# Kernel optimization log

Measured on AMD Instinct MI355X. Metric: run time of the kernel, lower is better.

The kernel has to match this reference:

```python
import jax, jax.numpy as jnp
import numpy as np

Q_LO, Q_HI = 0.15, 0.85   # quantiles from __init__ q=(0.15, 0.85)
Z_INDEX = 0.0             # Z_index=0 -> mask = outside [q_lo, q_hi]
Z_SIMPLE = 1.0            # Z_index_simple fallback


def _nn_diff(S1, S2):
    # For each point in S1, signed per-coordinate residual to its nearest
    # neighbor in S2 (brute-force cdist + argmin + gather). S1:[N,3] S2:[M,3]
    d2 = (jnp.sum(S1 * S1, -1)[:, None] + jnp.sum(S2 * S2, -1)[None, :]
          - 2.0 * (S1 @ S2.T))              # [N, M] squared distances
    idx = jnp.argmin(d2, axis=1)            # nearest index in S2, [N]
    return S1 - S2[idx]                     # [N, 3]


def _robust_masked_std(x):
    # torch: quantile-based outlier mask (no_grad), then unbiased std of
    # the masked elements. Implemented with mask weights so shapes are static.
    xf = x.reshape(-1)
    xs = jax.lax.stop_gradient(xf)
    qs = jnp.quantile(xs, jnp.array([Q_LO, Q_HI], dtype=xs.dtype))
    iqr = qs[1] - qs[0]
    mask = (xs < qs[0] - Z_INDEX * iqr) | (xs > qs[1] + Z_INDEX * iqr)
    # fallback chain matching torch edge cases: simple |x-mean|>Z*std, then all
    mu, sd = xs.mean(), xs.std(ddof=1)
    simple = jnp.abs(xs - mu) > Z_SIMPLE * sd
    simple = jnp.where(simple.sum() > 0, simple, jnp.ones_like(simple))
    w = jnp.where(mask.sum() > 0, mask, simple).astype(xf.dtype)
    cnt = w.sum()
    mean_w = jnp.sum(w * xf) / cnt
    var = jnp.sum(w * (xf - mean_w) ** 2) / (cnt - 1.0)  # unbiased (torch.std)
    return jnp.sqrt(var)


def _sigma_max(S1, S2):
    s1 = _robust_masked_std(_nn_diff(S1, S2))  # std of S1->S2 residuals
    s2 = _robust_masked_std(_nn_diff(S2, S1))  # std of S2->S1 residuals
    return jnp.maximum(s1, s2)                 # max(self.sigma_distance(...))


def setup_inputs() -> dict:
    key = jax.random.key(0)
    k1, k2 = jax.random.split(key)
    B, N, M, D = 16, 4096, 4096, 3
    x = jax.random.uniform(k1, (B, N, D), dtype=jnp.float32)
    y = jax.random.uniform(k2, (B, M, D), dtype=jnp.float32)
    return {"x": x, "y": y}


def reference(x, y):
    per_batch = jax.vmap(_sigma_max)(x, y)  # [B]
    return per_batch.mean()
```

## Files before the change

### kernel.cpp

```cpp
#include <hip/hip_runtime.h>
#include <stdint.h>
#include <math.h>

typedef unsigned short u16;
typedef unsigned long long ull;

#define NPTS  4096
#define NB    16
#define NRES  12288
#define NPAIR 32
#define G     16
#define NCELL 4096
#define HCEL  0.0625f
#define SSTR  4160
#define MARGIN 1e-5f
#define RANK_LO 1843u
#define RANK_HI 10443u

__device__ __forceinline__ uint32_t f2key(float f) {
    uint32_t u = __float_as_uint(f);
    return (u & 0x80000000u) ? ~u : (u | 0x80000000u);
}
__device__ __forceinline__ float key2f(uint32_t k) {
    uint32_t u = (k & 0x80000000u) ? (k ^ 0x80000000u) : ~k;
    return __uint_as_float(u);
}

__global__ __launch_bounds__(1024) void build_kernel(const float* __restrict__ x,
                                                     const float* __restrict__ y,
                                                     float4* __restrict__ arrA,
                                                     u16* __restrict__ starts,
                                                     u16* __restrict__ idx16,
                                                     unsigned int* __restrict__ counters) {
    __shared__ uint32_t hist[NCELL];
    __shared__ uint32_t wpart[16];
    const int pd = blockIdx.x, b = pd >> 1, dir = pd & 1;
    const float* t = (dir == 0 ? y : x) + (size_t)b * NPTS * 3;
    const int tid = threadIdx.x, lane = tid & 63, wv = tid >> 6;

    #pragma unroll
    for (int j = 0; j < 4; ++j) hist[tid * 4 + j] = 0u;
    if (pd == 0 && tid == 0) counters[0] = 0u;
    __syncthreads();

    float f[12];
    int ci[4];
    {
        const float4* tp = reinterpret_cast<const float4*>(t + (size_t)tid * 12);
        #pragma unroll
        for (int j = 0; j < 3; ++j) {
            const float4 v = tp[j];
            f[j * 4 + 0] = v.x; f[j * 4 + 1] = v.y; f[j * 4 + 2] = v.z; f[j * 4 + 3] = v.w;
        }
        #pragma unroll
        for (int k = 0; k < 4; ++k) {
            const int cx = (int)(f[k * 3 + 0] * 16.f);
            const int cy = (int)(f[k * 3 + 1] * 16.f);
            const int cz = (int)(f[k * 3 + 2] * 16.f);
            ci[k] = (cx * G + cy) * G + cz;
            atomicAdd(&hist[ci[k]], 1u);
        }
    }
    __syncthreads();

    {
        uint32_t loc[4], sum = 0;
        const int base = tid * 4;
        #pragma unroll
        for (int j = 0; j < 4; ++j) { loc[j] = hist[base + j]; sum += loc[j]; }
        uint32_t sc = sum;
        #pragma unroll
        for (int off = 1; off < 64; off <<= 1) {
            const uint32_t u = __shfl_up(sc, off);
            if (lane >= off) sc += u;
        }
        if (lane == 63) wpart[wv] = sc;
        __syncthreads();
        uint32_t wbase = 0;
        #pragma unroll
        for (int k = 0; k < 16; ++k) wbase += (k < wv) ? wpart[k] : 0u;
        uint32_t ex = wbase + sc - sum;
        #pragma unroll
        for (int j = 0; j < 4; ++j) { hist[base + j] = ex; ex += loc[j]; }
    }
    __syncthreads();

    for (int i = tid; i <= NCELL; i += 1024)
        starts[(size_t)pd * SSTR + i] = (u16)((i == NCELL) ? NPTS : hist[i]);
    __syncthreads();

    #pragma unroll
    for (int k = 0; k < 4; ++k) {
        const float px = f[k * 3 + 0], py = f[k * 3 + 1], pz = f[k * 3 + 2];
        const uint32_t pos = atomicAdd(&hist[ci[k]], 1u);
        const float w = fmaf(pz, pz, fmaf(py, py, px * px));
        arrA[(size_t)pd * NPTS + pos] = make_float4(-2.f * px, -2.f * py, -2.f * pz, w);
        idx16[(size_t)pd * NPTS + pos] = (u16)(tid * 4 + k);
    }
}

__global__ __launch_bounds__(256, 8) void query_kernel(const float4* __restrict__ arrA,
                                                       const u16* __restrict__ starts,
                                                       const u16* __restrict__ idx16,
                                                       uint32_t* __restrict__ keys,
                                                       double* __restrict__ partials) {
    __shared__ double wred[8];
    const int pd = blockIdx.y;
    const int tid = threadIdx.x, lane = tid & 63, wv = tid >> 6;
    const int l4 = tid & 3;
    const int p = blockIdx.x * 64 + (tid >> 2);

    const float4* __restrict__ tp = arrA + (size_t)pd * NPTS;
    const u16* __restrict__ st = starts + (size_t)pd * SSTR;
    const u16* __restrict__ ixp = idx16 + (size_t)pd * NPTS;

    const float4 Q = arrA[(size_t)(pd ^ 1) * NPTS + p];
    const float qx = -0.5f * Q.x, qy = -0.5f * Q.y, qz = -0.5f * Q.z;
    const float qq = Q.w;
    const int cx = (int)(qx * 16.f), cy = (int)(qy * 16.f), cz = (int)(qz * 16.f);

    float best = 3.0e38f;
    ull pk = ~0ull;

    #define SCAN_RUN(A_, E_)                                                        \
        for (int p2 = (A_) + l4; p2 < (E_); p2 += 4) {                              \
            const float4 T = tp[p2];                                                \
            const float d = fmaf(qx, T.x, fmaf(qy, T.y, fmaf(qz, T.z, T.w)));       \
            best = fminf(best, d);                                                  \
            const ull cand = ((ull)f2key(d) << 32) |                                \
                             ((ull)ixp[p2] << 16) | (uint32_t)p2;                   \
            pk = (cand < pk) ? cand : pk;                                           \
        }

    {
        const int zlo = max(cz - 1, 0), zhi = min(cz + 1, G - 1);
        int a9[9], e9[9];
        #pragma unroll
        for (int r = 0; r < 9; ++r) {
            const int ix = min(max(cx + (r / 3) - 1, 0), G - 1);
            const int iy = min(max(cy + (r % 3) - 1, 0), G - 1);
            const int c0 = (ix * G + iy) * G;
            a9[r] = st[c0 + zlo];
            e9[r] = st[c0 + zhi + 1];
        }
        #pragma unroll
        for (int r = 0; r < 9; ++r) SCAN_RUN(a9[r], e9[r])
    }

    for (int s = 2; s <= G - 1; ++s) {
        float qb = best;
        qb = fminf(qb, __shfl_xor(qb, 1));
        qb = fminf(qb, __shfl_xor(qb, 2));
        const float dmin = (float)(s - 1) * HCEL;
        if (fmaf(dmin, dmin, -(qb + qq)) > MARGIN) break;
        for (int dx = -s; dx <= s; ++dx) {
            const int ix = cx + dx;
            if (ix < 0 || ix > G - 1) continue;
            const int adx = dx < 0 ? -dx : dx;
            for (int dy = -s; dy <= s; ++dy) {
                const int iy = cy + dy;
                if (iy < 0 || iy > G - 1) continue;
                const int ady = dy < 0 ? -dy : dy;
                const int c0 = (ix * G + iy) * G;
                if (max(adx, ady) == s) {
                    const int zl = max(cz - s, 0), zh = min(cz + s, G - 1);
                    const int a = st[c0 + zl], e = st[c0 + zh + 1];
                    SCAN_RUN(a, e)
                } else {
                    const int z1 = cz - s;
                    if (z1 >= 0) { const int a = st[c0 + z1], e = st[c0 + z1 + 1]; SCAN_RUN(a, e) }
                    const int z2 = cz + s;
                    if (z2 <= G - 1) { const int a = st[c0 + z2], e = st[c0 + z2 + 1]; SCAN_RUN(a, e) }
                }
            }
        }
    }
    #undef SCAN_RUN

    {
        ull o = __shfl_xor(pk, 1); pk = (o < pk) ? o : pk;
        o = __shfl_xor(pk, 2);     pk = (o < pk) ? o : pk;
    }

    const int pos = (int)(pk & 0xFFFFull);
    const float4 T = tp[pos];
    const float rx = qx - (-0.5f * T.x);
    const float ry = qy - (-0.5f * T.y);
    const float rz = qz - (-0.5f * T.z);

    if (l4 < 3) {
        const uint32_t kk = (l4 == 0) ? f2key(rx) : ((l4 == 1) ? f2key(ry) : f2key(rz));
        keys[(size_t)pd * NRES + (size_t)p * 3 + l4] = kk;
    }

    double s1 = 0.0, s2 = 0.0;
    if (l4 == 0) {
        s1 = (double)rx + (double)ry + (double)rz;
        s2 = (double)rx * rx + (double)ry * ry + (double)rz * rz;
    }
    #pragma unroll
    for (int off = 32; off; off >>= 1) { s1 += __shfl_down(s1, off); s2 += __shfl_down(s2, off); }
    if (lane == 0) { wred[wv] = s1; wred[4 + wv] = s2; }
    __syncthreads();
    if (tid == 0) {
        double a = 0.0, c = 0.0;
        for (int k = 0; k < 4; ++k) { a += wred[k]; c += wred[4 + k]; }
        partials[(size_t)pd * 128 + blockIdx.x + 0]  = a;
        partials[(size_t)pd * 128 + 64 + blockIdx.x] = c;
    }
}

template <int BPT>
__device__ __forceinline__ void scanB(uint32_t* h, uint32_t* wtmp) {
    const int tid = threadIdx.x, lane = tid & 63, wv = tid >> 6;
    const int base = tid * BPT;
    uint32_t loc[BPT], sum = 0;
    #pragma unroll
    for (int j = 0; j < BPT; ++j) { loc[j] = h[base + j]; sum += loc[j]; }
    uint32_t sc = sum;
    #pragma unroll
    for (int off = 1; off < 64; off <<= 1) {
        const uint32_t u = __shfl_up(sc, off);
        if (lane >= off) sc += u;
    }
    if (lane == 63) wtmp[wv] = sc;
    __syncthreads();
    uint32_t wb = 0;
    #pragma unroll
    for (int k = 0; k < 16; ++k) wb += (k < wv) ? wtmp[k] : 0u;
    uint32_t ex = wb + sc - sum;
    #pragma unroll
    for (int j = 0; j < BPT; ++j) { h[base + j] = ex; ex += loc[j]; }
    __syncthreads();
}

template <int BPT>
__device__ __forceinline__ void psearchB(const uint32_t* h, int n, uint32_t r,
                                         uint32_t total, uint32_t* out3) {
    const int base = threadIdx.x * BPT;
    #pragma unroll
    for (int j = 0; j < BPT; ++j) {
        const int i = base + j;
        if (i < n) {
            const uint32_t lo = h[i];
            const uint32_t hi = (i + 1 < n) ? h[i + 1] : total;
            if (lo <= r && r < hi) { out3[0] = (uint32_t)i; out3[1] = lo; out3[2] = hi; }
        }
    }
}

__global__ __launch_bounds__(1024) void sigma_kernel(const uint32_t* __restrict__ keysg,
                                                     const double* __restrict__ partials,
                                                     float* __restrict__ sig,
                                                     unsigned int* __restrict__ counters,
                                                     float* __restrict__ out) {
    __shared__ uint32_t hist[4096];
    __shared__ uint32_t wtmp[16];
    __shared__ uint32_t bc[12];
    __shared__ double dr[64];
    __shared__ int io[32];
    __shared__ uint32_t um[32];

    const int pair = blockIdx.x;
    const int tid = threadIdx.x, lane = tid & 63, wv = tid >> 6;

    uint32_t key[12];
    const uint32_t* kp = keysg + (size_t)pair * NRES;
    #pragma unroll
    for (int e = 0; e < 12; ++e) key[e] = kp[e * 1024 + tid];

    {
        double a = (tid < 128) ? partials[(size_t)pair * 128 + tid] : 0.0;
        #pragma unroll
        for (int off = 32; off; off >>= 1) a += __shfl_down(a, off);
        if (lane == 0 && wv < 2) dr[wv] = a;
    }
    __syncthreads();
    const double S = dr[0], S2 = dr[1];
    const double mu = S / NRES;
    const double var_all = (S2 - S * mu) / (NRES - 1);
    const double sd = sqrt(var_all > 0.0 ? var_all : 0.0);
    __syncthreads();

    hist[tid * 2] = 0u; hist[tid * 2 + 1] = 0u;
    __syncthreads();
    #pragma unroll
    for (int e = 0; e < 12; ++e) atomicAdd(&hist[key[e] >> 21], 1u);
    __syncthreads();
    scanB<2>(hist, wtmp);
    psearchB<2>(hist, 2048, RANK_LO, NRES, bc + 0);
    psearchB<2>(hist, 2048, RANK_HI, NRES, bc + 3);
    __syncthreads();
    const uint32_t pA1 = bc[0], rA1 = RANK_LO - bc[1], totA1 = bc[2] - bc[1];
    const uint32_t pB1 = bc[3], rB1 = RANK_HI - bc[4], totB1 = bc[5] - bc[4];
    __syncthreads();

    #pragma unroll
    for (int j = 0; j < 4; ++j) hist[tid * 4 + j] = 0u;
    __syncthreads();
    #pragma unroll
    for (int e = 0; e < 12; ++e) {
        const uint32_t k = key[e];
        const uint32_t pfx = k >> 21, bin = (k >> 10) & 2047u;
        if (pfx == pA1) atomicAdd(&hist[bin], 1u);
        if (pfx == pB1) atomicAdd(&hist[2048 + bin], 1u);
    }
    __syncthreads();
    scanB<2>(hist, wtmp);
    scanB<2>(hist + 2048, wtmp);
    psearchB<2>(hist, 2048, rA1, totA1, bc + 0);
    psearchB<2>(hist + 2048, 2048, rB1, totB1, bc + 3);
    __syncthreads();
    const uint32_t pA2 = (pA1 << 11) | bc[0], rA2 = rA1 - bc[1], totA2 = bc[2] - bc[1];
    const uint32_t pB2 = (pB1 << 11) | bc[3], rB2 = rB1 - bc[4], totB2 = bc[5] - bc[4];
    __syncthreads();

    hist[tid * 2] = 0u; hist[tid * 2 + 1] = 0u;
    __syncthreads();
    #pragma unroll
    for (int e = 0; e < 12; ++e) {
        const uint32_t k = key[e];
        if ((k >> 10) == pA2) atomicAdd(&hist[k & 1023u], 1u);
        if ((k >> 10) == pB2) atomicAdd(&hist[1024 + (k & 1023u)], 1u);
    }
    __syncthreads();
    scanB<1>(hist, wtmp);
    scanB<1>(hist + 1024, wtmp);
    psearchB<1>(hist, 1024, rA2, totA2, bc + 0);
    psearchB<1>(hist + 1024, 1024, rB2, totB2, bc + 3);
    __syncthreads();
    const uint32_t k0 = (pA2 << 10) | bc[0];
    const uint32_t k2 = (pB2 << 10) | bc[3];
    const bool dup1 = (bc[2] >= rA2 + 2u);
    const bool dup3 = (bc[5] >= rB2 + 2u);

    uint32_t m1 = 0xFFFFFFFFu, m3 = 0xFFFFFFFFu;
    #pragma unroll
    for (int e = 0; e < 12; ++e) {
        const uint32_t k = key[e];
        if (k > k0 && k < m1) m1 = k;
        if (k > k2 && k < m3) m3 = k;
    }
    {
        uint32_t a = m1, c = m3;
        #pragma unroll
        for (int off = 32; off; off >>= 1) {
            const uint32_t ua = __shfl_down(a, off), uc = __shfl_down(c, off);
            a = (ua < a) ? ua : a; c = (uc < c) ? uc : c;
        }
        if (lane == 0) { um[wv] = a; um[16 + wv] = c; }
    }
    __syncthreads();
    uint32_t m1r = 0xFFFFFFFFu, m3r = 0xFFFFFFFFu;
    for (int k = 0; k < 16; ++k) {
        m1r = (um[k] < m1r) ? um[k] : m1r;
        m3r = (um[16 + k] < m3r) ? um[16 + k] : m3r;
    }
    const uint32_t k1 = dup1 ? k0 : m1r;
    const uint32_t k3 = dup3 ? k2 : m3r;

    const double vl0 = (double)key2f(k0), vl1 = (double)key2f(k1);
    const double vh0 = (double)key2f(k2), vh1 = (double)key2f(k3);
    const double fr_lo = 0.15 * (NRES - 1) - (double)RANK_LO;
    const double fr_hi = 0.85 * (NRES - 1) - (double)RANK_HI;
    const float q_lo = (float)(vl0 + fr_lo * (vl1 - vl0));
    const float q_hi = (float)(vh0 + fr_hi * (vh1 - vh0));

    int cq = 0, cs = 0;
    double sq = 0.0, ss = 0.0, sqq = 0.0, ssq = 0.0;
    #pragma unroll
    for (int e = 0; e < 12; ++e) {
        const float f = key2f(key[e]);
        const double fd = (double)f;
        if ((f < q_lo) || (f > q_hi)) { cq++; sq += fd; sqq += fd * fd; }
        if (fabs(fd - mu) > sd)       { cs++; ss += fd; ssq += fd * fd; }
    }
    {
        double a0 = sq, a1 = ss, a2 = sqq, a3 = ssq;
        int b0 = cq, b1 = cs;
        #pragma unroll
        for (int off = 32; off; off >>= 1) {
            a0 += __shfl_down(a0, off); a1 += __shfl_down(a1, off);
            a2 += __shfl_down(a2, off); a3 += __shfl_down(a3, off);
            b0 += __shfl_down(b0, off); b1 += __shfl_down(b1, off);
        }
        if (lane == 0) {
            dr[wv] = a0; dr[16 + wv] = a1; dr[32 + wv] = a2; dr[48 + wv] = a3;
            io[wv] = b0; io[16 + wv] = b1;
        }
    }
    __syncthreads();
    if (tid == 0) {
        double sq_t = 0, ss_t = 0, sqq_t = 0, ssq_t = 0;
        int cq_t = 0, cs_t = 0;
        for (int k = 0; k < 16; ++k) {
            sq_t += dr[k]; ss_t += dr[16 + k]; sqq_t += dr[32 + k]; ssq_t += dr[48 + k];
            cq_t += io[k]; cs_t += io[16 + k];
        }
        double cnt, sum, sumsq;
        if (cq_t > 0)      { cnt = cq_t;  sum = sq_t; sumsq = sqq_t; }
        else if (cs_t > 0) { cnt = cs_t;  sum = ss_t; sumsq = ssq_t; }
        else               { cnt = NRES;  sum = S;    sumsq = S2; }
        const double mean_w = sum / cnt;
        const double var = (sumsq - cnt * mean_w * mean_w) / (cnt - 1.0);
        const float sv = (float)sqrt(var > 0.0 ? var : 0.0);

        __hip_atomic_store(&sig[pair], sv, __ATOMIC_RELEASE, __HIP_MEMORY_SCOPE_AGENT);
        const unsigned prev = __hip_atomic_fetch_add(&counters[0], 1u,
                                                     __ATOMIC_ACQ_REL,
                                                     __HIP_MEMORY_SCOPE_AGENT);
        if (prev == NPAIR - 1) {
            float m = 0.f;
            for (int i = 0; i < NB; ++i) {
                const float s0 = __hip_atomic_load(&sig[2 * i], __ATOMIC_ACQUIRE,
                                                   __HIP_MEMORY_SCOPE_AGENT);
                const float s1v = __hip_atomic_load(&sig[2 * i + 1], __ATOMIC_ACQUIRE,
                                                    __HIP_MEMORY_SCOPE_AGENT);
                m += fmaxf(s0, s1v);
            }
            out[0] = m / (float)NB;
        }
    }
}

extern "C" void kernel_launch(void* const* d_in, const int* in_sizes, int n_in,
                              void* d_out, int out_size, void* d_ws, size_t ws_size,
                              hipStream_t stream) {
    const float* x = (const float*)d_in[0];
    const float* y = (const float*)d_in[1];
    char* w = (char*)d_ws;
    float4*       arrA     = (float4*)(w);
    uint32_t*     keys     = (uint32_t*)(w + 2097152);
    double*       partials = (double*)(w + 3670016);
    float*        sig      = (float*)(w + 3702784);
    unsigned int* counters = (unsigned int*)(w + 3702912);
    u16*          starts   = (u16*)(w + 3703040);
    u16*          idx16    = (u16*)(w + 3969280);

    build_kernel<<<NPAIR, 1024, 0, stream>>>(x, y, arrA, starts, idx16, counters);
    query_kernel<<<dim3(64, NPAIR), 256, 0, stream>>>(arrA, starts, idx16,
                                                      keys, partials);
    sigma_kernel<<<NPAIR, 1024, 0, stream>>>(keys, partials, sig, counters,
                                             (float*)d_out);
}
```

Measured before the change: 111.9 us.

## Flatten 3x3 neighbor runs into one strided loop and drop original-index tiebreak

```diff
diff --git a/kernel.cpp b/kernel.cpp
--- a/kernel.cpp
+++ b/kernel.cpp
@@ -30,7 +30,6 @@
                                                      const float* __restrict__ y,
                                                      float4* __restrict__ arrA,
                                                      u16* __restrict__ starts,
-                                                     u16* __restrict__ idx16,
                                                      unsigned int* __restrict__ counters) {
     __shared__ uint32_t hist[NCELL];
     __shared__ uint32_t wpart[16];
@@ -95,13 +94,11 @@
         const uint32_t pos = atomicAdd(&hist[ci[k]], 1u);
         const float w = fmaf(pz, pz, fmaf(py, py, px * px));
         arrA[(size_t)pd * NPTS + pos] = make_float4(-2.f * px, -2.f * py, -2.f * pz, w);
-        idx16[(size_t)pd * NPTS + pos] = (u16)(tid * 4 + k);
     }
 }
 
 __global__ __launch_bounds__(256, 8) void query_kernel(const float4* __restrict__ arrA,
                                                        const u16* __restrict__ starts,
-                                                       const u16* __restrict__ idx16,
                                                        uint32_t* __restrict__ keys,
                                                        double* __restrict__ partials) {
     __shared__ double wred[8];
@@ -112,47 +109,59 @@
 
     const float4* __restrict__ tp = arrA + (size_t)pd * NPTS;
     const u16* __restrict__ st = starts + (size_t)pd * SSTR;
-    const u16* __restrict__ ixp = idx16 + (size_t)pd * NPTS;
 
     const float4 Q = arrA[(size_t)(pd ^ 1) * NPTS + p];
     const float qx = -0.5f * Q.x, qy = -0.5f * Q.y, qz = -0.5f * Q.z;
     const float qq = Q.w;
     const int cx = (int)(qx * 16.f), cy = (int)(qy * 16.f), cz = (int)(qz * 16.f);
 
-    float best = 3.0e38f;
     ull pk = ~0ull;
 
-    #define SCAN_RUN(A_, E_)                                                        \
-        for (int p2 = (A_) + l4; p2 < (E_); p2 += 4) {                              \
-            const float4 T = tp[p2];                                                \
-            const float d = fmaf(qx, T.x, fmaf(qy, T.y, fmaf(qz, T.z, T.w)));       \
-            best = fminf(best, d);                                                  \
-            const ull cand = ((ull)f2key(d) << 32) |                                \
-                             ((ull)ixp[p2] << 16) | (uint32_t)p2;                   \
-            pk = (cand < pk) ? cand : pk;                                           \
-        }
-
     {
         const int zlo = max(cz - 1, 0), zhi = min(cz + 1, G - 1);
-        int a9[9], e9[9];
-        #pragma unroll
-        for (int r = 0; r < 9; ++r) {
-            const int ix = min(max(cx + (r / 3) - 1, 0), G - 1);
-            const int iy = min(max(cy + (r % 3) - 1, 0), G - 1);
-            const int c0 = (ix * G + iy) * G;
-            a9[r] = st[c0 + zlo];
-            e9[r] = st[c0 + zhi + 1];
-        }
-        #pragma unroll
-        for (int r = 0; r < 9; ++r) SCAN_RUN(a9[r], e9[r])
+        #define RUNB(RR, AV, NV)                                                  \
+            int AV, NV;                                                           \
+            { const int ix = min(max(cx + (RR) / 3 - 1, 0), G - 1);               \
+              const int iy = min(max(cy + (RR) % 3 - 1, 0), G - 1);               \
+              const int cc = (ix * G + iy) * G;                                   \
+              AV = st[cc + zlo];                                                  \
+              NV = st[cc + zhi + 1] - AV; }
+        RUNB(0, a0, n0) RUNB(1, a1, n1) RUNB(2, a2, n2)
+        RUNB(3, a3, n3) RUNB(4, a4, n4) RUNB(5, a5, n5)
+        RUNB(6, a6, n6) RUNB(7, a7, n7) RUNB(8, a8, n8)
+        #undef RUNB
+        const int nc = n0 + n1 + n2 + n3 + n4 + n5 + n6 + n7 + n8;
+
+        for (int li = l4; li < nc; li += 4) {
+            int pos;
+            {
+                int rem = li; pos = a0 + rem;
+                rem -= n0; pos = (rem >= 0) ? a1 + rem : pos;
+                rem -= n1; pos = (rem >= 0) ? a2 + rem : pos;
+                rem -= n2; pos = (rem >= 0) ? a3 + rem : pos;
+                rem -= n3; pos = (rem >= 0) ? a4 + rem : pos;
+                rem -= n4; pos = (rem >= 0) ? a5 + rem : pos;
+                rem -= n5; pos = (rem >= 0) ? a6 + rem : pos;
+                rem -= n6; pos = (rem >= 0) ? a7 + rem : pos;
+                rem -= n7; pos = (rem >= 0) ? a8 + rem : pos;
+                pos = min(pos, NPTS - 1);
+            }
+            const float4 T = tp[pos];
+            const float d = fmaf(qx, T.x, fmaf(qy, T.y, fmaf(qz, T.z, T.w)));
+            const ull cand = ((ull)f2key(d) << 32) | (uint32_t)pos;
+            pk = (cand < pk) ? cand : pk;
+        }
+    }
+
+    {
+        ull o = __shfl_xor(pk, 1); pk = (o < pk) ? o : pk;
+        o = __shfl_xor(pk, 2);     pk = (o < pk) ? o : pk;
     }
 
     for (int s = 2; s <= G - 1; ++s) {
-        float qb = best;
-        qb = fminf(qb, __shfl_xor(qb, 1));
-        qb = fminf(qb, __shfl_xor(qb, 2));
+        const float bd = key2f((uint32_t)(pk >> 32));
         const float dmin = (float)(s - 1) * HCEL;
-        if (fmaf(dmin, dmin, -(qb + qq)) > MARGIN) break;
+        if (fmaf(dmin, dmin, -(bd + qq)) > MARGIN) break;
         for (int dx = -s; dx <= s; ++dx) {
             const int ix = cx + dx;
             if (ix < 0 || ix > G - 1) continue;
@@ -162,27 +171,32 @@
                 if (iy < 0 || iy > G - 1) continue;
                 const int ady = dy < 0 ? -dy : dy;
                 const int c0 = (ix * G + iy) * G;
+                #define SCANS(A_, E_)                                                 \
+                    for (int p2 = (A_) + l4; p2 < (E_); p2 += 4) {                    \
+                        const float4 T = tp[p2];                                      \
+                        const float d = fmaf(qx, T.x, fmaf(qy, T.y,                   \
+                                             fmaf(qz, T.z, T.w)));                    \
+                        const ull cand = ((ull)f2key(d) << 32) | (uint32_t)p2;        \
+                        pk = (cand < pk) ? cand : pk;                                 \
+                    }
                 if (max(adx, ady) == s) {
                     const int zl = max(cz - s, 0), zh = min(cz + s, G - 1);
                     const int a = st[c0 + zl], e = st[c0 + zh + 1];
-                    SCAN_RUN(a, e)
+                    SCANS(a, e)
                 } else {
                     const int z1 = cz - s;
-                    if (z1 >= 0) { const int a = st[c0 + z1], e = st[c0 + z1 + 1]; SCAN_RUN(a, e) }
+                    if (z1 >= 0) { const int a = st[c0 + z1], e = st[c0 + z1 + 1]; SCANS(a, e) }
                     const int z2 = cz + s;
-                    if (z2 <= G - 1) { const int a = st[c0 + z2], e = st[c0 + z2 + 1]; SCAN_RUN(a, e) }
+                    if (z2 <= G - 1) { const int a = st[c0 + z2], e = st[c0 + z2 + 1]; SCANS(a, e) }
                 }
+                #undef SCANS
             }
         }
-    }
-    #undef SCAN_RUN
-
-    {
         ull o = __shfl_xor(pk, 1); pk = (o < pk) ? o : pk;
         o = __shfl_xor(pk, 2);     pk = (o < pk) ? o : pk;
     }
 
-    const int pos = (int)(pk & 0xFFFFull);
+    const int pos = (int)(uint32_t)pk;
     const float4 T = tp[pos];
     const float rx = qx - (-0.5f * T.x);
     const float ry = qy - (-0.5f * T.y);
@@ -435,11 +449,9 @@
     float*        sig      = (float*)(w + 3702784);
     unsigned int* counters = (unsigned int*)(w + 3702912);
     u16*          starts   = (u16*)(w + 3703040);
-    u16*          idx16    = (u16*)(w + 3969280);
-
-    build_kernel<<<NPAIR, 1024, 0, stream>>>(x, y, arrA, starts, idx16, counters);
-    query_kernel<<<dim3(64, NPAIR), 256, 0, stream>>>(arrA, starts, idx16,
-                                                      keys, partials);
+
+    build_kernel<<<NPAIR, 1024, 0, stream>>>(x, y, arrA, starts, counters);
+    query_kernel<<<dim3(64, NPAIR), 256, 0, stream>>>(arrA, starts, keys, partials);
     sigma_kernel<<<NPAIR, 1024, 0, stream>>>(keys, partials, sig, counters,
                                              (float*)d_out);
 }
```

New measurement: 109.0 us. 2.6% less time.
